# Kernel optimization log

Measured on AMD Instinct MI355X. Metric: run time of the kernel, lower is better.

## Reference

```python
import jax, jax.numpy as jnp
import numpy as np

# STN forward: grid = reference_ijk_grid + ddf (voxel units); the module then
# normalizes each axis to [-1,1] with align_corners=True and reverses axis order
# for F.grid_sample. Under align_corners=True the normalize->denormalize round
# trip is the identity, so the sample locations are exactly ref+ddf in voxel
# coordinates per (d,h,w) axis. padding_mode='border' => clamp coords to the
# valid range before trilinear interpolation.

def _grid_sample_3d_border(image, ddf):
    # image: [B,C,D,H,W], ddf: [B,3,D,H,W] (voxel-space displacements in d,h,w order)
    B, C, D, H, W = image.shape
    dt = image.dtype
    ref = jnp.stack(
        jnp.meshgrid(jnp.arange(D, dtype=dt), jnp.arange(H, dtype=dt),
                     jnp.arange(W, dtype=dt), indexing='ij'), axis=0)  # [3,D,H,W]
    coords = ref[None] + ddf  # [B,3,D,H,W] absolute voxel coords

    def sample_one(img, c):  # img [C,D,H,W], c [3,D,H,W]
        cd = jnp.clip(c[0], 0.0, D - 1.0)  # border padding: clamp coord
        ch = jnp.clip(c[1], 0.0, H - 1.0)
        cw = jnp.clip(c[2], 0.0, W - 1.0)
        d0 = jnp.floor(cd); h0 = jnp.floor(ch); w0 = jnp.floor(cw)
        fd = cd - d0; fh = ch - h0; fw = cw - w0  # [D,H,W] fractional weights
        d0i = d0.astype(jnp.int32); h0i = h0.astype(jnp.int32); w0i = w0.astype(jnp.int32)
        d1i = jnp.minimum(d0i + 1, D - 1)
        h1i = jnp.minimum(h0i + 1, H - 1)
        w1i = jnp.minimum(w0i + 1, W - 1)

        def g(di, hi, wi):  # gather 1 corner for all channels -> [C,D,H,W]
            return img[:, di, hi, wi]

        out = (g(d0i, h0i, w0i) * ((1 - fd) * (1 - fh) * (1 - fw))
             + g(d0i, h0i, w1i) * ((1 - fd) * (1 - fh) * fw)
             + g(d0i, h1i, w0i) * ((1 - fd) * fh * (1 - fw))
             + g(d0i, h1i, w1i) * ((1 - fd) * fh * fw)
             + g(d1i, h0i, w0i) * (fd * (1 - fh) * (1 - fw))
             + g(d1i, h0i, w1i) * (fd * (1 - fh) * fw)
             + g(d1i, h1i, w0i) * (fd * fh * (1 - fw))
             + g(d1i, h1i, w1i) * (fd * fh * fw))
        return out

    return jax.vmap(sample_one)(image, coords)  # [B,C,D,H,W]


def setup_inputs() -> dict:
    key = jax.random.key(0)
    k1, k2 = jax.random.split(key)
    image = jax.random.normal(k1, (2, 2, 128, 128, 128), dtype=jnp.float32)
    ddf = jax.random.normal(k2, (2, 3, 128, 128, 128), dtype=jnp.float32)
    return {"image": image, "ddf": ddf}


def reference(image, ddf):
    return _grid_sample_3d_border(image, ddf)
```

## Files before the change

### kernel.cpp

```cpp
#include <hip/hip_runtime.h>


constexpr int B = 2, C = 2, D = 128, H = 128, W = 128;
constexpr int HW  = H * W;
constexpr int DHW = D * HW;
constexpr int RD = 11, RH = 15;
constexpr int ROWD = 44;
constexpr int GPR = 11;
constexpr int NROWR = RD * RH;
constexpr int NG = 2048;
constexpr int NT = 512;
constexpr int ROW_B = ROWD * 4;
constexpr int PLANE_B = RH * ROW_B;

typedef float v2f __attribute__((ext_vector_type(2)));

__device__ __forceinline__ void gload_lds16(const float* g, float* l) {
    __builtin_amdgcn_global_load_lds(
        (const __attribute__((address_space(1))) void*)g,
        (__attribute__((address_space(3))) void*)l, 16, 0, 0);
}

__global__ __launch_bounds__(NT) void stn_kernel(
    const float* __restrict__ image,
    const float* __restrict__ ddf,
    float* __restrict__ out)
{
    __shared__ float smem[NG * 4];

    const int bid = blockIdx.x;
    const int cpx = gridDim.x >> 3;
    const int blk = (bid & 7) * cpx + (bid >> 3);

    const int b  = blk >> 11;
    const int tb = blk & 2047;
    const int t0d = (tb >> 6) * 4;
    const int t0h = ((tb >> 2) & 15) * 8;
    const int t0w = (tb & 3) * 32;
    const int lo_d = max(t0d - 3, 0), lo_h = max(t0h - 3, 0);
    const int lo_w = max(t0w - 4, 0);
    const int hi_d = min(lo_d + RD - 1, D - 1);
    const int hi_h = min(lo_h + RH - 1, H - 1);
    const int hi_w = min(lo_w + 39, W - 1);
    const float* imgb = image + (size_t)b * C * DHW;
    const int tid = threadIdx.x;
    const unsigned lds0 =
        (unsigned)(uintptr_t)(__attribute__((address_space(3))) void*)&smem[0];

    const int dd = tid >> 7, hh = (tid >> 4) & 7, wi = tid & 15;
    const int d_ = t0d + dd, h_ = t0h + hh;
    const int w2 = t0w + wi * 2;
    const int sidx = d_ * HW + h_ * W + w2;

    const float* dp = ddf + (size_t)b * 3 * DHW;
    float2 vd = *reinterpret_cast<const float2*>(dp + sidx);
    float2 vh = *reinterpret_cast<const float2*>(dp + DHW + sidx);
    float2 vw = *reinterpret_cast<const float2*>(dp + 2 * DHW + sidx);
    asm volatile("" ::: "memory");

    auto gsrc_off = [&](int g) {
        int row = g / GPR;
        int rw  = (g - row * GPR) * 4;
        int rc  = min(row, NROWR - 1);
        int rd  = rc / RH;
        int rh  = rc - rd * RH;
        return min(lo_d + rd, D - 1) * HW + min(lo_h + rh, H - 1) * W
             + min(lo_w + rw, W - 4);
    };

    auto issue_stage = [&](const float* src) {
#pragma unroll
        for (int i = 0; i < 4; ++i) {
            int g = tid + i * NT;
            gload_lds16(src + gsrc_off(g), &smem[g * 4]);
        }
    };

    issue_stage(imgb);
    asm volatile("" ::: "memory");

    float cds[2], chs[2], cws[2];
    cds[0] = fminf(fmaxf((float)d_ + vd.x, 0.0f), (float)(D - 1));
    cds[1] = fminf(fmaxf((float)d_ + vd.y, 0.0f), (float)(D - 1));
    chs[0] = fminf(fmaxf((float)h_ + vh.x, 0.0f), (float)(H - 1));
    chs[1] = fminf(fmaxf((float)h_ + vh.y, 0.0f), (float)(H - 1));
    cws[0] = fminf(fmaxf((float)w2 + vw.x, 0.0f), (float)(W - 1));
    cws[1] = fminf(fmaxf((float)(w2 + 1) + vw.y, 0.0f), (float)(W - 1));

    unsigned a0[2];
    float W00[2], W01[2], W10[2], W11[2], GD[2], FD[2];
    int fb = 0;
#pragma unroll
    for (int k = 0; k < 2; ++k) {
        float cd = cds[k], ch = chs[k], cw = cws[k];
        float d0f = floorf(cd), h0f = floorf(ch), w0f = floorf(cw);
        float fd = cd - d0f, fh = ch - h0f, fw = cw - w0f;
        int d0 = (int)d0f, h0 = (int)h0f, w0 = (int)w0f;
        bool bad = (d0 < lo_d) | (d0 + 1 > hi_d)
                 | (h0 < lo_h) | (h0 + 1 > hi_h)
                 | (w0 < lo_w) | (w0 + 1 > hi_w);
        fb |= (int)bad << k;
        float gh = 1.0f - fh, gw = 1.0f - fw;
        W00[k] = gh * gw; W01[k] = gh * fw;
        W10[k] = fh * gw; W11[k] = fh * fw;
        GD[k] = 1.0f - fd; FD[k] = fd;
        int row = (d0 - lo_d) * RH + (h0 - lo_h);
        a0[k] = lds0 + (unsigned)(row * ROW_B + (w0 - lo_w) * 4);
    }

    auto do_pass = [&](const float* gimg, float* optr) {
        v2f r00[2], r01[2], r10[2], r11[2];
#pragma unroll
        for (int k = 0; k < 2; ++k) {
            unsigned a1 = a0[k] + PLANE_B;
            asm volatile("ds_read2_b32 %0, %1 offset0:0 offset1:1"
                         : "=v"(r00[k]) : "v"(a0[k]));
            asm volatile("ds_read2_b32 %0, %1 offset0:44 offset1:45"
                         : "=v"(r01[k]) : "v"(a0[k]));
            asm volatile("ds_read2_b32 %0, %1 offset0:0 offset1:1"
                         : "=v"(r10[k]) : "v"(a1));
            asm volatile("ds_read2_b32 %0, %1 offset0:44 offset1:45"
                         : "=v"(r11[k]) : "v"(a1));
        }
        asm volatile("s_waitcnt lgkmcnt(0)" ::: "memory");
        __builtin_amdgcn_sched_barrier(0);

        float acc[2];
#pragma unroll
        for (int k = 0; k < 2; ++k) {
            float p0 = r00[k].x * W00[k] + r00[k].y * W01[k]
                     + r01[k].x * W10[k] + r01[k].y * W11[k];
            float p1 = r10[k].x * W00[k] + r10[k].y * W01[k]
                     + r11[k].x * W10[k] + r11[k].y * W11[k];
            acc[k] = GD[k] * p0 + FD[k] * p1;
        }
        if (fb) {
#pragma unroll
            for (int k = 0; k < 2; ++k) {
                if (fb & (1 << k)) {
                    float cd = cds[k], ch = chs[k], cw = cws[k];
                    float d0f = floorf(cd), h0f = floorf(ch), w0f = floorf(cw);
                    float fd = cd - d0f, fh = ch - h0f, fw = cw - w0f;
                    int d0 = (int)d0f, h0 = (int)h0f, w0 = (int)w0f;
                    int d1 = min(d0 + 1, D - 1);
                    int h1 = min(h0 + 1, H - 1);
                    int w1 = min(w0 + 1, W - 1);
                    float gd = 1.0f - fd, gh = 1.0f - fh, gw = 1.0f - fw;
                    float w00 = gh * gw, w01 = gh * fw, w10 = fh * gw, w11 = fh * fw;
                    int o00 = d0 * HW + h0 * W, o01 = d0 * HW + h1 * W;
                    int o10 = d1 * HW + h0 * W, o11 = d1 * HW + h1 * W;
                    float q0 = gimg[o00 + w0] * w00 + gimg[o00 + w1] * w01
                             + gimg[o01 + w0] * w10 + gimg[o01 + w1] * w11;
                    float q1 = gimg[o10 + w0] * w00 + gimg[o10 + w1] * w01
                             + gimg[o11 + w0] * w10 + gimg[o11 + w1] * w11;
                    acc[k] = gd * q0 + fd * q1;
                }
            }
        }
        *reinterpret_cast<float2*>(optr) = make_float2(acc[0], acc[1]);
    };

    float* outb = out + (size_t)b * C * DHW;

    asm volatile("s_waitcnt vmcnt(0)" ::: "memory");
    __builtin_amdgcn_s_barrier();
    do_pass(imgb, outb + sidx);

    __builtin_amdgcn_s_barrier();
    asm volatile("" ::: "memory");

    issue_stage(imgb + DHW);
    asm volatile("s_waitcnt vmcnt(0)" ::: "memory");
    __builtin_amdgcn_s_barrier();
    do_pass(imgb + DHW, outb + DHW + sidx);
}

extern "C" void kernel_launch(void* const* d_in, const int* in_sizes, int n_in,
                              void* d_out, int out_size, void* d_ws, size_t ws_size,
                              hipStream_t stream) {
    const float* image = (const float*)d_in[0];
    const float* ddf   = (const float*)d_in[1];
    float* out = (float*)d_out;

    int grid = B * 2048;
    stn_kernel<<<grid, NT, 0, stream>>>(image, ddf, out);
}
```

Baseline: 35.30 us.

## Double output tile depth per block to improve LDS halo reuse

Each block now covers an 8x8x32 output tile instead of 4x8x32, so every thread computes four voxels (two h rows) per channel. The LDS halo region grows from 11 to 15 depth planes, which lowers the halo-to-interior ratio and cuts redundant image loads. A tail of groups past 4*NT is loaded with ordinary float4 loads and LDS stores, so the waits now also cover lgkmcnt. The grid is halved, which means fewer blocks for latency hiding, along with more LDS per block and more registers per thread.

Measured after the change: 41.84 us. 18.5% more time.

```diff
diff --git a/kernel.cpp b/kernel.cpp
--- a/kernel.cpp
+++ b/kernel.cpp
@@ -4,12 +4,13 @@
 constexpr int B = 2, C = 2, D = 128, H = 128, W = 128;
 constexpr int HW  = H * W;
 constexpr int DHW = D * HW;
-constexpr int RD = 11, RH = 15;
+constexpr int RD = 15, RH = 15;
 constexpr int ROWD = 44;
 constexpr int GPR = 11;
 constexpr int NROWR = RD * RH;
-constexpr int NG = 2048;
+constexpr int NGR = NROWR * GPR;
 constexpr int NT = 512;
+constexpr int TAILN = NGR - 4 * NT;
 constexpr int ROW_B = ROWD * 4;
 constexpr int PLANE_B = RH * ROW_B;
 
@@ -26,15 +27,15 @@
     const float* __restrict__ ddf,
     float* __restrict__ out)
 {
-    __shared__ float smem[NG * 4];
+    __shared__ float smem[NROWR * ROWD];
 
     const int bid = blockIdx.x;
     const int cpx = gridDim.x >> 3;
     const int blk = (bid & 7) * cpx + (bid >> 3);
 
-    const int b  = blk >> 11;
-    const int tb = blk & 2047;
-    const int t0d = (tb >> 6) * 4;
+    const int b  = blk >> 10;
+    const int tb = blk & 1023;
+    const int t0d = (tb >> 6) * 8;
     const int t0h = ((tb >> 2) & 15) * 8;
     const int t0w = (tb & 3) * 32;
     const int lo_d = max(t0d - 3, 0), lo_h = max(t0h - 3, 0);
@@ -47,15 +48,20 @@
     const unsigned lds0 =
         (unsigned)(uintptr_t)(__attribute__((address_space(3))) void*)&smem[0];
 
-    const int dd = tid >> 7, hh = (tid >> 4) & 7, wi = tid & 15;
-    const int d_ = t0d + dd, h_ = t0h + hh;
+    const int dl = tid >> 6, hl = (tid >> 4) & 3, wi = tid & 15;
+    const int d_ = t0d + dl;
+    const int h0_ = t0h + hl;
     const int w2 = t0w + wi * 2;
-    const int sidx = d_ * HW + h_ * W + w2;
+    const int sidx0 = d_ * HW + h0_ * W + w2;
+    const int sidx1 = sidx0 + 4 * W;
 
     const float* dp = ddf + (size_t)b * 3 * DHW;
-    float2 vd = *reinterpret_cast<const float2*>(dp + sidx);
-    float2 vh = *reinterpret_cast<const float2*>(dp + DHW + sidx);
-    float2 vw = *reinterpret_cast<const float2*>(dp + 2 * DHW + sidx);
+    float2 vd0 = *reinterpret_cast<const float2*>(dp + sidx0);
+    float2 vd1 = *reinterpret_cast<const float2*>(dp + sidx1);
+    float2 vh0 = *reinterpret_cast<const float2*>(dp + DHW + sidx0);
+    float2 vh1 = *reinterpret_cast<const float2*>(dp + DHW + sidx1);
+    float2 vw0 = *reinterpret_cast<const float2*>(dp + 2 * DHW + sidx0);
+    float2 vw1 = *reinterpret_cast<const float2*>(dp + 2 * DHW + sidx1);
     asm volatile("" ::: "memory");
 
     auto gsrc_off = [&](int g) {
@@ -74,71 +80,82 @@
             int g = tid + i * NT;
             gload_lds16(src + gsrc_off(g), &smem[g * 4]);
         }
+        if (tid < TAILN) {
+            int g = tid + 4 * NT;
+            float4 v = *reinterpret_cast<const float4*>(src + gsrc_off(g));
+            *reinterpret_cast<float4*>(&smem[g * 4]) = v;
+        }
     };
 
     issue_stage(imgb);
     asm volatile("" ::: "memory");
 
-    float cds[2], chs[2], cws[2];
-    cds[0] = fminf(fmaxf((float)d_ + vd.x, 0.0f), (float)(D - 1));
-    cds[1] = fminf(fmaxf((float)d_ + vd.y, 0.0f), (float)(D - 1));
-    chs[0] = fminf(fmaxf((float)h_ + vh.x, 0.0f), (float)(H - 1));
-    chs[1] = fminf(fmaxf((float)h_ + vh.y, 0.0f), (float)(H - 1));
-    cws[0] = fminf(fmaxf((float)w2 + vw.x, 0.0f), (float)(W - 1));
-    cws[1] = fminf(fmaxf((float)(w2 + 1) + vw.y, 0.0f), (float)(W - 1));
-
-    unsigned a0[2];
-    float W00[2], W01[2], W10[2], W11[2], GD[2], FD[2];
-    int fb = 0;
-#pragma unroll
-    for (int k = 0; k < 2; ++k) {
-        float cd = cds[k], ch = chs[k], cw = cws[k];
-        float d0f = floorf(cd), h0f = floorf(ch), w0f = floorf(cw);
-        float fd = cd - d0f, fh = ch - h0f, fw = cw - w0f;
-        int d0 = (int)d0f, h0 = (int)h0f, w0 = (int)w0f;
-        bool bad = (d0 < lo_d) | (d0 + 1 > hi_d)
-                 | (h0 < lo_h) | (h0 + 1 > hi_h)
-                 | (w0 < lo_w) | (w0 + 1 > hi_w);
-        fb |= (int)bad << k;
-        float gh = 1.0f - fh, gw = 1.0f - fw;
-        W00[k] = gh * gw; W01[k] = gh * fw;
-        W10[k] = fh * gw; W11[k] = fh * fw;
-        GD[k] = 1.0f - fd; FD[k] = fd;
-        int row = (d0 - lo_d) * RH + (h0 - lo_h);
-        a0[k] = lds0 + (unsigned)(row * ROW_B + (w0 - lo_w) * 4);
+    float cds[4], chs[4], cws[4];
+    {
+        const float ad[4] = {vd0.x, vd0.y, vd1.x, vd1.y};
+        const float ah[4] = {vh0.x, vh0.y, vh1.x, vh1.y};
+        const float aw[4] = {vw0.x, vw0.y, vw1.x, vw1.y};
+#pragma unroll
+        for (int v = 0; v < 4; ++v) {
+            int hv = h0_ + (v >> 1) * 4;
+            int wv = w2 + (v & 1);
+            cds[v] = fminf(fmaxf((float)d_ + ad[v], 0.0f), (float)(D - 1));
+            chs[v] = fminf(fmaxf((float)hv + ah[v], 0.0f), (float)(H - 1));
+            cws[v] = fminf(fmaxf((float)wv + aw[v], 0.0f), (float)(W - 1));
+        }
     }
 
-    auto do_pass = [&](const float* gimg, float* optr) {
-        v2f r00[2], r01[2], r10[2], r11[2];
-#pragma unroll
-        for (int k = 0; k < 2; ++k) {
-            unsigned a1 = a0[k] + PLANE_B;
+    auto do_pass = [&](const float* gimg, float* obase) {
+        unsigned a0[4];
+        float W00[4], W01[4], W10[4], W11[4], GD[4], FD[4];
+        int fb = 0;
+#pragma unroll
+        for (int v = 0; v < 4; ++v) {
+            float cd = cds[v], ch = chs[v], cw = cws[v];
+            float d0f = floorf(cd), h0f = floorf(ch), w0f = floorf(cw);
+            float fd = cd - d0f, fh = ch - h0f, fw = cw - w0f;
+            int d0 = (int)d0f, h0 = (int)h0f, w0 = (int)w0f;
+            bool bad = (d0 < lo_d) | (d0 + 1 > hi_d)
+                     | (h0 < lo_h) | (h0 + 1 > hi_h)
+                     | (w0 < lo_w) | (w0 + 1 > hi_w);
+            fb |= (int)bad << v;
+            float gh = 1.0f - fh, gw = 1.0f - fw;
+            W00[v] = gh * gw; W01[v] = gh * fw;
+            W10[v] = fh * gw; W11[v] = fh * fw;
+            GD[v] = 1.0f - fd; FD[v] = fd;
+            int row = (d0 - lo_d) * RH + (h0 - lo_h);
+            a0[v] = lds0 + (unsigned)(row * ROW_B + (w0 - lo_w) * 4);
+        }
+        v2f r00[4], r01[4], r10[4], r11[4];
+#pragma unroll
+        for (int v = 0; v < 4; ++v) {
+            unsigned a1 = a0[v] + PLANE_B;
             asm volatile("ds_read2_b32 %0, %1 offset0:0 offset1:1"
-                         : "=v"(r00[k]) : "v"(a0[k]));
+                         : "=v"(r00[v]) : "v"(a0[v]));
             asm volatile("ds_read2_b32 %0, %1 offset0:44 offset1:45"
-                         : "=v"(r01[k]) : "v"(a0[k]));
+                         : "=v"(r01[v]) : "v"(a0[v]));
             asm volatile("ds_read2_b32 %0, %1 offset0:0 offset1:1"
-                         : "=v"(r10[k]) : "v"(a1));
+                         : "=v"(r10[v]) : "v"(a1));
             asm volatile("ds_read2_b32 %0, %1 offset0:44 offset1:45"
-                         : "=v"(r11[k]) : "v"(a1));
+                         : "=v"(r11[v]) : "v"(a1));
         }
         asm volatile("s_waitcnt lgkmcnt(0)" ::: "memory");
         __builtin_amdgcn_sched_barrier(0);
 
-        float acc[2];
-#pragma unroll
-        for (int k = 0; k < 2; ++k) {
-            float p0 = r00[k].x * W00[k] + r00[k].y * W01[k]
-                     + r01[k].x * W10[k] + r01[k].y * W11[k];
-            float p1 = r10[k].x * W00[k] + r10[k].y * W01[k]
-                     + r11[k].x * W10[k] + r11[k].y * W11[k];
-            acc[k] = GD[k] * p0 + FD[k] * p1;
+        float acc[4];
+#pragma unroll
+        for (int v = 0; v < 4; ++v) {
+            float p0 = r00[v].x * W00[v] + r00[v].y * W01[v]
+                     + r01[v].x * W10[v] + r01[v].y * W11[v];
+            float p1 = r10[v].x * W00[v] + r10[v].y * W01[v]
+                     + r11[v].x * W10[v] + r11[v].y * W11[v];
+            acc[v] = GD[v] * p0 + FD[v] * p1;
         }
         if (fb) {
 #pragma unroll
-            for (int k = 0; k < 2; ++k) {
-                if (fb & (1 << k)) {
-                    float cd = cds[k], ch = chs[k], cw = cws[k];
+            for (int v = 0; v < 4; ++v) {
+                if (fb & (1 << v)) {
+                    float cd = cds[v], ch = chs[v], cw = cws[v];
                     float d0f = floorf(cd), h0f = floorf(ch), w0f = floorf(cw);
                     float fd = cd - d0f, fh = ch - h0f, fw = cw - w0f;
                     int d0 = (int)d0f, h0 = (int)h0f, w0 = (int)w0f;
@@ -153,26 +170,27 @@
                              + gimg[o01 + w0] * w10 + gimg[o01 + w1] * w11;
                     float q1 = gimg[o10 + w0] * w00 + gimg[o10 + w1] * w01
                              + gimg[o11 + w0] * w10 + gimg[o11 + w1] * w11;
-                    acc[k] = gd * q0 + fd * q1;
+                    acc[v] = gd * q0 + fd * q1;
                 }
             }
         }
-        *reinterpret_cast<float2*>(optr) = make_float2(acc[0], acc[1]);
+        *reinterpret_cast<float2*>(obase + sidx0) = make_float2(acc[0], acc[1]);
+        *reinterpret_cast<float2*>(obase + sidx1) = make_float2(acc[2], acc[3]);
     };
 
     float* outb = out + (size_t)b * C * DHW;
 
-    asm volatile("s_waitcnt vmcnt(0)" ::: "memory");
+    asm volatile("s_waitcnt vmcnt(0) lgkmcnt(0)" ::: "memory");
     __builtin_amdgcn_s_barrier();
-    do_pass(imgb, outb + sidx);
+    do_pass(imgb, outb);
 
     __builtin_amdgcn_s_barrier();
     asm volatile("" ::: "memory");
 
     issue_stage(imgb + DHW);
-    asm volatile("s_waitcnt vmcnt(0)" ::: "memory");
+    asm volatile("s_waitcnt vmcnt(0) lgkmcnt(0)" ::: "memory");
     __builtin_amdgcn_s_barrier();
-    do_pass(imgb + DHW, outb + DHW + sidx);
+    do_pass(imgb + DHW, outb + DHW);
 }
 
 extern "C" void kernel_launch(void* const* d_in, const int* in_sizes, int n_in,
@@ -182,6 +200,6 @@
     const float* ddf   = (const float*)d_in[1];
     float* out = (float*)d_out;
 
-    int grid = B * 2048;
+    int grid = B * 1024;
     stn_kernel<<<grid, NT, 0, stream>>>(image, ddf, out);
 }
```
